# Kernel tuning notes

Measured on AMD Instinct MI355X. Metric: run time of the kernel, lower is better.

The kernel has to match this reference:

```python
import jax, jax.numpy as jnp
import numpy as np
import math

H = 1024
N = 64          # d_state; complex modes = N // 2
N2 = N // 2
B = 8
L = 2048
DT_MIN, DT_MAX = 0.001, 0.1


def setup_inputs() -> dict:
    key = jax.random.key(0)
    ks = jax.random.split(key, 8)
    u = jax.random.normal(ks[0], (B, H, L), dtype=jnp.float32)
    # log_dt ~ Uniform[log(dt_min), log(dt_max)]
    log_dt = (jax.random.uniform(ks[1], (H,), dtype=jnp.float32)
              * (math.log(DT_MAX) - math.log(DT_MIN)) + math.log(DT_MIN))
    # random_dplr with scaling='inverse': real part 0.5, imag = (1/pi)*N*(N/(1+2n)-1)
    n = jnp.arange(N2, dtype=jnp.float32)
    w_real = 0.5 * jnp.ones((1, N2), dtype=jnp.float32)
    w_imag = ((1.0 / math.pi) * N * (N / (1.0 + 2.0 * n) - 1.0))[None, :].astype(jnp.float32)
    log_w_real = jnp.log(w_real + 1e-4)  # module stores log(-w.real + 1e-4)
    # C = randn complex (channels=1, H, N2), scaled by normalized B (folded into randn here)
    C_re = jax.random.normal(ks[2], (1, H, N2), dtype=jnp.float32) / math.sqrt(2 * N2)
    C_im = jax.random.normal(ks[3], (1, H, N2), dtype=jnp.float32) / math.sqrt(2 * N2)
    D = jax.random.normal(ks[4], (1, H), dtype=jnp.float32)
    # output_linear: Conv1d(k=1) from channels*H -> H  => weight (H, H)
    W_out = jax.random.normal(ks[5], (H, H), dtype=jnp.float32) / math.sqrt(H)
    b_out = jax.random.normal(ks[6], (H,), dtype=jnp.float32) * 0.01
    return {"u": u, "log_dt": log_dt, "log_w_real": log_w_real, "w_imag": w_imag,
            "C_re": C_re, "C_im": C_im, "D": D, "W_out": W_out, "b_out": b_out}


def reference(u, log_dt, log_w_real, w_imag, C_re, C_im, D, W_out, b_out):
    b, h, l = u.shape
    # --- SSKernelDiag.forward ---
    dt = jnp.exp(log_dt)                                   # (H,)
    w = -jnp.exp(log_w_real) + 1j * w_imag                 # (n_ssm=1, N2)
    w = jnp.broadcast_to(w, (h, w.shape[-1]))              # repeat copies -> (H, N2)
    dtA = w * dt[:, None]                                  # (H, N2) complex
    C = (C_re + 1j * C_im) * (jnp.exp(dtA) - 1.0) / w      # (c, H, N2)
    # Vandermonde: exp(dtA * arange(L)) -> (H, N2, L) complex
    K = jnp.exp(dtA[:, :, None] * jnp.arange(l, dtype=jnp.float32))
    k = 2.0 * jnp.einsum('chn,hnl->chl', C, K).real        # (c, H, L) float
    # --- FFT convolution ---
    k_f = jnp.fft.rfft(k, n=2 * l)                         # (c, H, L+1)
    u_f = jnp.fft.rfft(u, n=2 * l)                         # (B, H, L+1)
    y_f = jnp.einsum('bhl,chl->bchl', u_f, k_f)
    y = jnp.fft.irfft(y_f, n=2 * l)[..., :l]               # (B, c, H, L)
    # skip connection with D
    y = y + jnp.einsum('bhl,ch->bchl', u, D)
    y = y.reshape(b, -1, l)                                # (B, c*H, L)
    y = jax.nn.gelu(y, approximate=False)
    # output 1x1 conv: (B, c*H, L) x (H, c*H) -> (B, H, L)
    y = jnp.einsum('bil,oi->bol', y, W_out) + b_out[None, :, None]
    return y
```

## Files before the change

### kernel.cpp

```cpp
#include <hip/hip_runtime.h>
#include <hip/hip_bf16.h>

#define HH 1024
#define LL 2048
#define BB 8
#define NN2 32
#define CT 128
#define NCH 16

typedef short bf16x8 __attribute__((ext_vector_type(8)));
typedef float f32x4  __attribute__((ext_vector_type(4)));
typedef float f32x16 __attribute__((ext_vector_type(16)));

static __device__ __forceinline__ unsigned short bfbits(float x) {
    __hip_bfloat16 h = __float2bfloat16(x);
    return *(unsigned short*)&h;
}
static __device__ __forceinline__ float f_from_bits(unsigned short b) {
    __hip_bfloat16 h; *(unsigned short*)&h = b; return __bfloat162float(h);
}
static __device__ __forceinline__ float2 cexp_n(float2 dA, float p) {
    float mag = __expf(dA.x * p);
    float rev = dA.y * p * 0.15915494309f;
    rev -= floorf(rev);
    float ang = rev * 6.28318530718f;
    return make_float2(mag * __cosf(ang), mag * __sinf(ang));
}

#define SWZ(off, row) ((off) ^ (((row) & 7) << 4))

__global__ __launch_bounds__(256) void aux_tables(
    const float* __restrict__ log_dt, const float* __restrict__ log_w_real,
    const float* __restrict__ w_imag, const float* __restrict__ C_re,
    const float* __restrict__ C_im, const float* __restrict__ W,
    __hip_bfloat16* __restrict__ AJ_g, __hip_bfloat16* __restrict__ AP_g,
    float* __restrict__ misc_g, __hip_bfloat16* __restrict__ Wb)
{
    __shared__ float2 dtA_s[NN2];
    __shared__ float2 Cn_s[NN2];
    const int tid = threadIdx.x;
    const int h = blockIdx.x;

    {
        float4 v = ((const float4*)(W + (size_t)h * HH))[tid];
        ushort4 o;
        o.x = bfbits(v.x); o.y = bfbits(v.y); o.z = bfbits(v.z); o.w = bfbits(v.w);
        ((ushort4*)(Wb + (size_t)h * HH))[tid] = o;
    }

    if (tid < NN2) {
        int n = tid;
        float dt = expf(log_dt[h]);
        float wr = -expf(log_w_real[n]);
        float wi = w_imag[n];
        float dar = wr * dt, dai = wi * dt;
        dtA_s[n] = make_float2(dar, dai);
        float er = expf(dar);
        float sn, cs; sincosf(dai, &sn, &cs);
        float exr = er * cs - 1.0f, exi = er * sn;
        float den = wr * wr + wi * wi;
        float fr = (exr * wr + exi * wi) / den;
        float fi = (exi * wr - exr * wi) / den;
        float cre = C_re[h * NN2 + n], cim = C_im[h * NN2 + n];
        float2 Cv = make_float2(cre * fr - cim * fi, cre * fi + cim * fr);
        Cn_s[n] = Cv;
        misc_g[h * 256 + 128 + 2 * n]     = Cv.x;
        misc_g[h * 256 + 128 + 2 * n + 1] = Cv.y;
        float magA = expf(dar * 128.0f);
        float snA, csA; sincosf(dai * 128.0f, &snA, &csA);
        misc_g[h * 256 + 192 + 2 * n]     = magA * csA;
        misc_g[h * 256 + 192 + 2 * n + 1] = magA * snA;
    }
    __syncthreads();

    char* ajb = (char*)AJ_g + (size_t)h * 16384;
    #pragma unroll
    for (int q = 0; q < 2; ++q) {
        int task = q * 256 + tid;
        int n = task >> 4, j0 = (task & 15) * 8;
        float2 dA = dtA_s[n];
        unsigned rw[4], iw[4];
        #pragma unroll
        for (int i2 = 0; i2 < 4; ++i2) {
            float2 a0 = cexp_n(dA, (float)(127 - j0 - 2 * i2));
            float2 a1 = cexp_n(dA, (float)(127 - j0 - 2 * i2 - 1));
            rw[i2] = (unsigned)bfbits(a0.x) | ((unsigned)bfbits(a1.x) << 16);
            iw[i2] = (unsigned)bfbits(a0.y) | ((unsigned)bfbits(a1.y) << 16);
        }
        int r0 = 2 * n, r1 = 2 * n + 1;
        *(uint4*)(ajb + SWZ(r0 * 256 + j0 * 2, r0)) = make_uint4(rw[0], rw[1], rw[2], rw[3]);
        *(uint4*)(ajb + SWZ(r1 * 256 + j0 * 2, r1)) = make_uint4(iw[0], iw[1], iw[2], iw[3]);
    }

    char* apb = (char*)AP_g + (size_t)h * 16384;
    #pragma unroll
    for (int q = 0; q < 2; ++q) {
        int task = q * 256 + tid;
        int ttr = task >> 2, n0 = (task & 3) * 8;
        unsigned w[8];
        #pragma unroll
        for (int i = 0; i < 8; ++i) {
            float2 a = cexp_n(dtA_s[n0 + i], (float)(ttr + 1));
            w[i] = (unsigned)bfbits(2.0f * a.x) | ((unsigned)bfbits(-2.0f * a.y) << 16);
        }
        *(uint4*)(apb + SWZ(ttr * 128 + n0 * 4, ttr))      = make_uint4(w[0], w[1], w[2], w[3]);
        *(uint4*)(apb + SWZ(ttr * 128 + n0 * 4 + 16, ttr)) = make_uint4(w[4], w[5], w[6], w[7]);
    }

    {
        int t = tid >> 1, nb = (tid & 1) * 16;
        float s = 0.f;
        #pragma unroll
        for (int i = 0; i < 16; ++i) {
            int n = nb + i;
            float2 a = cexp_n(dtA_s[n], (float)t);
            float2 C = Cn_s[n];
            s += C.x * a.x - C.y * a.y;
        }
        s += __shfl_xor(s, 1);
        if ((tid & 1) == 0) misc_g[h * 256 + t] = 2.0f * s;
    }
}

#define S_U    0
#define S_UN   16384
#define S_P    32768
#define S_KT   40960
#define S_KTP  41984
#define S_TOT  46208

__global__ __launch_bounds__(512, 6) void ssm_mfma(
    const float* __restrict__ u,
    const __hip_bfloat16* __restrict__ AJ_g,
    const __hip_bfloat16* __restrict__ AP_g,
    const float* __restrict__ misc_g,
    const float* __restrict__ Dp, __hip_bfloat16* __restrict__ g_out)
{
    extern __shared__ char smem[];
    float*  kt   = (float*)(smem + S_KT);
    float2* CnL  = (float2*)(smem + S_KT + 512);
    float2* A128 = (float2*)(smem + S_KT + 768);

    const int tid  = threadIdx.x;
    const int lane = tid & 63;
    const int wave = tid >> 6;
    const int wm   = wave >> 2;
    const int wn   = wave & 3;
    const int h    = blockIdx.x;
    const int bh   = blockIdx.y;

    {
        const char* ajs = (const char*)AJ_g + (size_t)h * 16384;
        __builtin_amdgcn_global_load_lds(
            (const __attribute__((address_space(1))) void*)(ajs + tid * 16),
            (__attribute__((address_space(3))) void*)(smem + S_UN + wave * 1024), 16, 0, 0);
        __builtin_amdgcn_global_load_lds(
            (const __attribute__((address_space(1))) void*)(ajs + 8192 + tid * 16),
            (__attribute__((address_space(3))) void*)(smem + S_UN + 8192 + wave * 1024), 16, 0, 0);
        if (tid < 64) {
            const char* ms = (const char*)misc_g + (size_t)h * 1024;
            __builtin_amdgcn_global_load_lds(
                (const __attribute__((address_space(1))) void*)(ms + tid * 16),
                (__attribute__((address_space(3))) void*)(smem + S_KT), 16, 0, 0);
        }
    }

    float4 ureg[4];
    #pragma unroll
    for (int q = 0; q < 4; ++q) {
        int b = bh * 4 + q;
        ureg[q] = *(const float4*)(u + ((size_t)(b * HH + h)) * LL + tid * 4);
    }
    #pragma unroll
    for (int q = 0; q < 4; ++q) {
        int row = q * 16 + (tid >> 5);
        int j   = (tid & 31) * 4;
        ushort4 o;
        o.x = bfbits(ureg[q].x); o.y = bfbits(ureg[q].y);
        o.z = bfbits(ureg[q].z); o.w = bfbits(ureg[q].w);
        *(ushort4*)(smem + SWZ(S_U + row * 256 + j * 2, row)) = o;
    }
    asm volatile("s_waitcnt vmcnt(0)" ::: "memory");
    __syncthreads();

    {
        int s = wave;
        int i0 = lane * 4;
        ushort4 o;
        #pragma unroll
        for (int k = 0; k < 4; ++k) {
            int src = 127 - s - (i0 + k);
            ((unsigned short*)&o)[k] = (src >= 0) ? bfbits(kt[src]) : (unsigned short)0;
        }
        *(ushort4*)(smem + S_KTP + s * 528 + i0 * 2) = o;
        if (lane < 2) {
            *(ushort4*)(smem + S_KTP + s * 528 + 512 + lane * 8) = make_ushort4(0, 0, 0, 0);
        }
    }

    f32x4 accP[2] = {};
    #pragma unroll
    for (int ks = 0; ks < 4; ++ks) {
        int kf = ks * 32 + (lane >> 4) * 8;
        bf16x8 a0, a1, b0;
        {
            int r = wm * 32 + (lane & 15);
            a0 = *(bf16x8*)(smem + SWZ(S_U + r * 256 + kf * 2, r));
            int r2 = r + 16;
            a1 = *(bf16x8*)(smem + SWZ(S_U + r2 * 256 + kf * 2, r2));
        }
        {
            int r = wn * 16 + (lane & 15);
            b0 = *(bf16x8*)(smem + SWZ(S_UN + r * 256 + kf * 2, r));
        }
        accP[0] = __builtin_amdgcn_mfma_f32_16x16x32_bf16(a0, b0, accP[0], 0, 0, 0);
        accP[1] = __builtin_amdgcn_mfma_f32_16x16x32_bf16(a1, b0, accP[1], 0, 0, 0);
    }
    #pragma unroll
    for (int mt = 0; mt < 2; ++mt)
        #pragma unroll
        for (int r = 0; r < 4; ++r) {
            int row = wm * 32 + mt * 16 + (lane >> 4) * 4 + r;
            int col = wn * 16 + (lane & 15);
            *(unsigned short*)(smem + SWZ(S_P + row * 128 + col * 2, row)) =
                bfbits(accP[mt][r]);
        }
    __syncthreads();

    {
        const char* aps = (const char*)AP_g + (size_t)h * 16384;
        __builtin_amdgcn_global_load_lds(
            (const __attribute__((address_space(1))) void*)(aps + tid * 16),
            (__attribute__((address_space(3))) void*)(smem + S_UN + wave * 1024), 16, 0, 0);
        __builtin_amdgcn_global_load_lds(
            (const __attribute__((address_space(1))) void*)(aps + 8192 + tid * 16),
            (__attribute__((address_space(3))) void*)(smem + S_UN + 8192 + wave * 1024), 16, 0, 0);
    }

    if (tid < 128) {
        int b = tid >> 5, n = tid & 31;
        float2 C = CnL[n];
        float2 A = A128[n];
        unsigned int pv[NCH];
        int offs[NCH];
        #pragma unroll
        for (int c = 0; c < NCH; ++c) {
            int row = b * 16 + c;
            offs[c] = SWZ(S_P + row * 128 + n * 4, row);
            pv[c] = *(unsigned int*)(smem + offs[c]);
        }
        float sr = 0.f, si = 0.f;
        #pragma unroll
        for (int c = 0; c < NCH; ++c) {
            float pr = f_from_bits((unsigned short)(pv[c] & 0xffff));
            float pi = f_from_bits((unsigned short)(pv[c] >> 16));
            float csr = C.x * sr - C.y * si;
            float csi = C.x * si + C.y * sr;
            *(unsigned int*)(smem + offs[c]) =
                (unsigned)bfbits(csr) | ((unsigned)bfbits(csi) << 16);
            float nsr = A.x * sr - A.y * si + pr;
            float nsi = A.x * si + A.y * sr + pi;
            sr = nsr; si = nsi;
        }
    }

    f32x4 acc[2][2] = {};
    #pragma unroll
    for (int ks = 0; ks < 4; ++ks) {
        int kf = ks * 32 + (lane >> 4) * 8;
        bf16x8 a0, a1, bv[2];
        {
            int r = wm * 32 + (lane & 15);
            a0 = *(bf16x8*)(smem + SWZ(S_U + r * 256 + kf * 2, r));
            int r2 = r + 16;
            a1 = *(bf16x8*)(smem + SWZ(S_U + r2 * 256 + kf * 2, r2));
        }
        #pragma unroll
        for (int nt = 0; nt < 2; ++nt) {
            int ttr = wn * 32 + nt * 16 + (lane & 15);
            int s   = (127 - ttr) & 7;
            int gq  = (127 - ttr + kf) >> 3;
            bv[nt] = *(bf16x8*)(smem + S_KTP + s * 528 + gq * 16);
        }
        #pragma unroll
        for (int nt = 0; nt < 2; ++nt) {
            acc[0][nt] = __builtin_amdgcn_mfma_f32_16x16x32_bf16(a0, bv[nt], acc[0][nt], 0, 0, 0);
            acc[1][nt] = __builtin_amdgcn_mfma_f32_16x16x32_bf16(a1, bv[nt], acc[1][nt], 0, 0, 0);
        }
    }
    asm volatile("s_waitcnt vmcnt(0)" ::: "memory");
    __syncthreads();

    #pragma unroll
    for (int ks = 0; ks < 2; ++ks) {
        int kf = ks * 32 + (lane >> 4) * 8;
        bf16x8 a0, a1, bv[2];
        {
            int r = wm * 32 + (lane & 15);
            a0 = *(bf16x8*)(smem + SWZ(S_P + r * 128 + kf * 2, r));
            int r2 = r + 16;
            a1 = *(bf16x8*)(smem + SWZ(S_P + r2 * 128 + kf * 2, r2));
        }
        #pragma unroll
        for (int nt = 0; nt < 2; ++nt) {
            int ttr = wn * 32 + nt * 16 + (lane & 15);
            bv[nt] = *(bf16x8*)(smem + SWZ(S_UN + ttr * 128 + kf * 2, ttr));
        }
        #pragma unroll
        for (int nt = 0; nt < 2; ++nt) {
            acc[0][nt] = __builtin_amdgcn_mfma_f32_16x16x32_bf16(a0, bv[nt], acc[0][nt], 0, 0, 0);
            acc[1][nt] = __builtin_amdgcn_mfma_f32_16x16x32_bf16(a1, bv[nt], acc[1][nt], 0, 0, 0);
        }
    }

    const float Dv = Dp[h];
    #pragma unroll
    for (int mt = 0; mt < 2; ++mt)
        #pragma unroll
        for (int nt = 0; nt < 2; ++nt)
            #pragma unroll
            for (int r = 0; r < 4; ++r) {
                int row = wm * 32 + mt * 16 + (lane >> 4) * 4 + r;
                int ttr = wn * 32 + nt * 16 + (lane & 15);
                int off = SWZ(S_U + row * 256 + ttr * 2, row);
                float uv = f_from_bits(*(unsigned short*)(smem + off));
                float y = acc[mt][nt][r] + Dv * uv;
                float z = 0.7978845608f * (y + 0.044715f * y * y * y);
                float e = __expf(2.0f * z);
                float th = 1.0f - 2.0f / (e + 1.0f);
                float gel = 0.5f * y * (1.0f + th);
                *(unsigned short*)(smem + off) = bfbits(gel);
            }
    __syncthreads();
    #pragma unroll
    for (int q = 0; q < 2; ++q) {
        int flat = q * 512 + tid;
        int row = flat >> 4, c16 = flat & 15;
        uint4 v = *(uint4*)(smem + SWZ(S_U + row * 256 + c16 * 16, row));
        int b = bh * 4 + (row >> 4), c = row & 15;
        *(uint4*)(g_out + ((size_t)(b * HH + h)) * LL + c * CT + c16 * 8) = v;
    }
}

__global__ __launch_bounds__(256) void transpose_g(
    const __hip_bfloat16* __restrict__ g, __hip_bfloat16* __restrict__ gT)
{
    __shared__ __hip_bfloat16 t[64][66];
    const int tid = threadIdx.x;
    const int b  = blockIdx.z;
    const int h0 = blockIdx.x * 64;
    const int l0 = blockIdx.y * 64;

    #pragma unroll
    for (int q = 0; q < 2; ++q) {
        int idx = tid + q * 256;
        int r = idx >> 3, c8 = (idx & 7) * 8;
        uint4 v = *(const uint4*)(g + ((size_t)(b * HH + h0 + r)) * LL + l0 + c8);
        unsigned int* dst = (unsigned int*)&t[r][c8];
        dst[0] = v.x; dst[1] = v.y; dst[2] = v.z; dst[3] = v.w;
    }
    __syncthreads();
    #pragma unroll
    for (int q = 0; q < 2; ++q) {
        int idx = tid + q * 256;
        int r = idx >> 3, c8 = (idx & 7) * 8;
        unsigned short tmp[8];
        #pragma unroll
        for (int j = 0; j < 8; ++j) tmp[j] = *(unsigned short*)&t[c8 + j][r];
        uint4 o;
        o.x = (unsigned)tmp[0] | ((unsigned)tmp[1] << 16);
        o.y = (unsigned)tmp[2] | ((unsigned)tmp[3] << 16);
        o.z = (unsigned)tmp[4] | ((unsigned)tmp[5] << 16);
        o.w = (unsigned)tmp[6] | ((unsigned)tmp[7] << 16);
        *(uint4*)(gT + ((size_t)(b * LL + l0 + r)) * HH + h0 + c8) = o;
    }
}

#define GSLOT 32768
#define STAGE_TILE(kt_, s_)                                                      \
    {                                                                            \
        const int k0_ = (kt_) * 64;                                              \
        _Pragma("unroll")                                                        \
        for (int v_ = 0; v_ < 4; ++v_) {                                         \
            int row_ = v_ * 64 + rsub;                                           \
            const __hip_bfloat16* ga_ = Wb + (size_t)(o0 + row_) * HH + k0_ + csw; \
            const __hip_bfloat16* gb_ = gT + (size_t)(n0 + row_) * HH + k0_ + csw; \
            char* dA_ = smem + (s_) * GSLOT + (v_ * 64 + wave * 8) * 128;        \
            char* dB_ = smem + 2 * GSLOT + (s_) * GSLOT + (v_ * 64 + wave * 8) * 128; \
            __builtin_amdgcn_global_load_lds(                                    \
                (const __attribute__((address_space(1))) void*)ga_,              \
                (__attribute__((address_space(3))) void*)dA_, 16, 0, 0);         \
            __builtin_amdgcn_global_load_lds(                                    \
                (const __attribute__((address_space(1))) void*)gb_,              \
                (__attribute__((address_space(3))) void*)dB_, 16, 0, 0);         \
        }                                                                        \
    }

#define COMPUTE_TILE(s_)                                                         \
    {                                                                            \
        const char* baseA = smem + (s_) * GSLOT;                                 \
        const char* baseB = smem + 2 * GSLOT + (s_) * GSLOT;                     \
        _Pragma("unroll")                                                        \
        for (int ks = 0; ks < 4; ++ks) {                                         \
            int kf = ks * 16 + (lane >> 5) * 8;                                  \
            bf16x8 af[4], bfv[2];                                                \
            _Pragma("unroll")                                                    \
            for (int mt = 0; mt < 4; ++mt) {                                     \
                int ra = wm * 128 + mt * 32 + (lane & 31);                       \
                int c  = kf ^ ((ra & 7) << 3);                                   \
                af[mt] = *(const bf16x8*)(baseA + ra * 128 + c * 2);             \
            }                                                                    \
            _Pragma("unroll")                                                    \
            for (int nt = 0; nt < 2; ++nt) {                                     \
                int rb = wn * 64 + nt * 32 + (lane & 31);                        \
                int c  = kf ^ ((rb & 7) << 3);                                   \
                bfv[nt] = *(const bf16x8*)(baseB + rb * 128 + c * 2);            \
            }                                                                    \
            _Pragma("unroll")                                                    \
            for (int mt = 0; mt < 4; ++mt)                                       \
                _Pragma("unroll")                                                \
                for (int nt = 0; nt < 2; ++nt)                                   \
                    acc[mt][nt] = __builtin_amdgcn_mfma_f32_32x32x16_bf16(       \
                        af[mt], bfv[nt], acc[mt][nt], 0, 0, 0);                  \
        }                                                                        \
    }

__global__ __launch_bounds__(512, 2) void out_gemm_256(
    const __hip_bfloat16* __restrict__ Wb,
    const __hip_bfloat16* __restrict__ gT,
    const float* __restrict__ bias,
    float* __restrict__ out)
{
    extern __shared__ char smem[];
    const int tid  = threadIdx.x;
    const int lane = tid & 63;
    const int wave = tid >> 6;
    const int wm = wave >> 2;
    const int wn = wave & 3;

    int wg  = blockIdx.x;
    int swz = (wg & 7) * 32 + (wg >> 3);
    const int o0 = (swz & 3) * 256;
    const int n0 = (swz >> 2) * 256;

    const int rsub = tid >> 3;
    const int csw  = ((tid & 7) ^ (rsub & 7)) << 3;

    f32x16 acc[4][2] = {};

    STAGE_TILE(0, 0)
    STAGE_TILE(1, 1)

    for (int t = 0; t < 15; ++t) {
        asm volatile("s_waitcnt vmcnt(8)" ::: "memory");
        __builtin_amdgcn_s_barrier();
        COMPUTE_TILE(t & 1)
        asm volatile("s_waitcnt lgkmcnt(0)" ::: "memory");
        __builtin_amdgcn_s_barrier();
        if (t < 14) STAGE_TILE(t + 2, t & 1)
    }
    asm volatile("s_waitcnt vmcnt(0)" ::: "memory");
    __builtin_amdgcn_s_barrier();
    COMPUTE_TILE(1)

    const int bb = n0 >> 11;
    #pragma unroll
    for (int mt = 0; mt < 4; ++mt) {
        int obase = o0 + wm * 128 + mt * 32 + 4 * (lane >> 5);
        #pragma unroll
        for (int nt = 0; nt < 2; ++nt) {
            int l = (n0 + wn * 64 + nt * 32 + (lane & 31)) & 2047;
            #pragma unroll
            for (int reg = 0; reg < 16; ++reg) {
                int o = obase + (reg & 3) + 8 * (reg >> 2);
                out[((size_t)(bb * HH + o)) * LL + l] = acc[mt][nt][reg] + bias[o];
            }
        }
    }
}

extern "C" void kernel_launch(void* const* d_in, const int* in_sizes, int n_in,
                              void* d_out, int out_size, void* d_ws, size_t ws_size,
                              hipStream_t stream) {
    const float* u          = (const float*)d_in[0];
    const float* log_dt     = (const float*)d_in[1];
    const float* log_w_real = (const float*)d_in[2];
    const float* w_imag     = (const float*)d_in[3];
    const float* C_re       = (const float*)d_in[4];
    const float* C_im       = (const float*)d_in[5];
    const float* Dp         = (const float*)d_in[6];
    const float* W          = (const float*)d_in[7];
    const float* bias       = (const float*)d_in[8];
    float* out = (float*)d_out;

    __hip_bfloat16* AJ_g = (__hip_bfloat16*)d_out;
    __hip_bfloat16* AP_g = (__hip_bfloat16*)((char*)d_out + 16777216);
    __hip_bfloat16* g    = (__hip_bfloat16*)((char*)d_out + 33554432);
    __hip_bfloat16* gT     = (__hip_bfloat16*)d_ws;
    __hip_bfloat16* Wb     = (__hip_bfloat16*)((char*)d_ws + 33554432);
    float*          misc_g = (float*)((char*)d_ws + 35651584);

    hipFuncSetAttribute((const void*)ssm_mfma,
                        hipFuncAttributeMaxDynamicSharedMemorySize, S_TOT);
    hipFuncSetAttribute((const void*)out_gemm_256,
                        hipFuncAttributeMaxDynamicSharedMemorySize, 131072);

    aux_tables<<<dim3(HH), 256, 0, stream>>>(log_dt, log_w_real, w_imag,
                                             C_re, C_im, W, AJ_g, AP_g, misc_g, Wb);
    ssm_mfma<<<dim3(HH, 2), 512, S_TOT, stream>>>(u, AJ_g, AP_g, misc_g, Dp, g);
    transpose_g<<<dim3(HH / 64, LL / 64, BB), 256, 0, stream>>>(g, gT);
    out_gemm_256<<<dim3(256), 512, 131072, stream>>>(Wb, gT, bias, out);
}
```

Before: 101.9 us.

## Move GELU into transpose and restructure output GEMM into quadrant-pipelined 16x16 MFMA

GELU moves out of the SSM kernel's epilogue and into the transpose kernel, so the SSM kernel writes the pre-activation value. The output GEMM drops 32x32x16 MFMAs in favour of 16x16x32 ones and splits each 256x256 tile into four quadrants. Staging of the next K-tile's A/B halves is interleaved between quadrant MFMA phases with finer vmcnt waits. The aim is to overlap global-to-LDS loads with compute and to ease SSM-kernel work. The cost is more barriers per tile and a different register footprint, since the launch bound drops its min-blocks hint and may cut occupancy.

```diff
diff --git a/kernel.cpp b/kernel.cpp
--- a/kernel.cpp
+++ b/kernel.cpp
@@ -10,7 +10,6 @@
 
 typedef short bf16x8 __attribute__((ext_vector_type(8)));
 typedef float f32x4  __attribute__((ext_vector_type(4)));
-typedef float f32x16 __attribute__((ext_vector_type(16)));
 
 static __device__ __forceinline__ unsigned short bfbits(float x) {
     __hip_bfloat16 h = __float2bfloat16(x);
@@ -25,6 +24,11 @@
     rev -= floorf(rev);
     float ang = rev * 6.28318530718f;
     return make_float2(mag * __cosf(ang), mag * __sinf(ang));
+}
+static __device__ __forceinline__ float gelu_f(float y) {
+    float z = 0.7978845608f * (y + 0.044715f * y * y * y);
+    float e = __expf(2.0f * z);
+    return 0.5f * y * (1.0f + (1.0f - 2.0f / (e + 1.0f)));
 }
 
 #define SWZ(off, row) ((off) ^ (((row) & 7) << 4))
@@ -325,11 +329,7 @@
                 int off = SWZ(S_U + row * 256 + ttr * 2, row);
                 float uv = f_from_bits(*(unsigned short*)(smem + off));
                 float y = acc[mt][nt][r] + Dv * uv;
-                float z = 0.7978845608f * (y + 0.044715f * y * y * y);
-                float e = __expf(2.0f * z);
-                float th = 1.0f - 2.0f / (e + 1.0f);
-                float gel = 0.5f * y * (1.0f + th);
-                *(unsigned short*)(smem + off) = bfbits(gel);
+                *(unsigned short*)(smem + off) = bfbits(y);
             }
     __syncthreads();
     #pragma unroll
@@ -357,7 +357,14 @@
         int r = idx >> 3, c8 = (idx & 7) * 8;
         uint4 v = *(const uint4*)(g + ((size_t)(b * HH + h0 + r)) * LL + l0 + c8);
         unsigned int* dst = (unsigned int*)&t[r][c8];
-        dst[0] = v.x; dst[1] = v.y; dst[2] = v.z; dst[3] = v.w;
+        unsigned int* src = (unsigned int*)&v;
+        #pragma unroll
+        for (int w = 0; w < 4; ++w) {
+            unsigned int pw = src[w];
+            float a = gelu_f(f_from_bits((unsigned short)(pw & 0xffff)));
+            float c = gelu_f(f_from_bits((unsigned short)(pw >> 16)));
+            dst[w] = (unsigned)bfbits(a) | ((unsigned)bfbits(c) << 16);
+        }
     }
     __syncthreads();
     #pragma unroll
@@ -376,56 +383,99 @@
     }
 }
 
-#define GSLOT 32768
-#define STAGE_TILE(kt_, s_)                                                      \
+#define QSLOT 65536
+
+#define STAGE_A_HALF(kt_, s_, h_)                                                \
     {                                                                            \
         const int k0_ = (kt_) * 64;                                              \
         _Pragma("unroll")                                                        \
-        for (int v_ = 0; v_ < 4; ++v_) {                                         \
+        for (int v2_ = 0; v2_ < 2; ++v2_) {                                      \
+            int v_ = (h_) * 2 + v2_;                                             \
             int row_ = v_ * 64 + rsub;                                           \
             const __hip_bfloat16* ga_ = Wb + (size_t)(o0 + row_) * HH + k0_ + csw; \
-            const __hip_bfloat16* gb_ = gT + (size_t)(n0 + row_) * HH + k0_ + csw; \
-            char* dA_ = smem + (s_) * GSLOT + (v_ * 64 + wave * 8) * 128;        \
-            char* dB_ = smem + 2 * GSLOT + (s_) * GSLOT + (v_ * 64 + wave * 8) * 128; \
+            char* dA_ = smem + (s_) * QSLOT + (v_ * 64 + wave * 8) * 128;        \
             __builtin_amdgcn_global_load_lds(                                    \
                 (const __attribute__((address_space(1))) void*)ga_,              \
                 (__attribute__((address_space(3))) void*)dA_, 16, 0, 0);         \
+        }                                                                        \
+    }
+
+#define STAGE_B_HALF(kt_, s_, h_)                                                \
+    {                                                                            \
+        const int k0_ = (kt_) * 64;                                              \
+        _Pragma("unroll")                                                        \
+        for (int v2_ = 0; v2_ < 2; ++v2_) {                                      \
+            int v_ = (h_) * 2 + v2_;                                             \
+            int row_ = v_ * 64 + rsub;                                           \
+            const __hip_bfloat16* gb_ = gT + (size_t)(n0 + row_) * HH + k0_ + csw; \
+            char* dB_ = smem + (s_) * QSLOT + 32768 + (v_ * 64 + wave * 8) * 128; \
             __builtin_amdgcn_global_load_lds(                                    \
                 (const __attribute__((address_space(1))) void*)gb_,              \
                 (__attribute__((address_space(3))) void*)dB_, 16, 0, 0);         \
         }                                                                        \
     }
 
-#define COMPUTE_TILE(s_)                                                         \
+#define READ_A(af_, qa_)                                                         \
+    _Pragma("unroll")                                                            \
+    for (int mt = 0; mt < 2; ++mt)                                               \
+        _Pragma("unroll")                                                        \
+        for (int ks = 0; ks < 2; ++ks) {                                         \
+            int ra = (qa_) * 128 + wm4 * 32 + mt * 16 + (lane & 15);             \
+            int c  = (ks * 32 + (lane >> 4) * 8) ^ ((ra & 7) << 3);              \
+            af_[mt][ks] = *(const bf16x8*)(baseA + ra * 128 + c * 2);            \
+        }
+
+#define READ_B(bf_, qb_)                                                         \
+    _Pragma("unroll")                                                            \
+    for (int nt = 0; nt < 4; ++nt)                                               \
+        _Pragma("unroll")                                                        \
+        for (int ks = 0; ks < 2; ++ks) {                                         \
+            int rb = (qb_) * 128 + wn2 * 64 + nt * 16 + (lane & 15);             \
+            int c  = (ks * 32 + (lane >> 4) * 8) ^ ((rb & 7) << 3);              \
+            bf_[nt][ks] = *(const bf16x8*)(baseB + rb * 128 + c * 2);            \
+        }
+
+#define DO_MFMA(qa_, qb_, af_, bf_)                                              \
+    _Pragma("unroll")                                                            \
+    for (int mt = 0; mt < 2; ++mt)                                               \
+        _Pragma("unroll")                                                        \
+        for (int nt = 0; nt < 4; ++nt) {                                         \
+            acc[qa_][qb_][mt][nt] = __builtin_amdgcn_mfma_f32_16x16x32_bf16(     \
+                af_[mt][0], bf_[nt][0], acc[qa_][qb_][mt][nt], 0, 0, 0);         \
+            acc[qa_][qb_][mt][nt] = __builtin_amdgcn_mfma_f32_16x16x32_bf16(     \
+                af_[mt][1], bf_[nt][1], acc[qa_][qb_][mt][nt], 0, 0, 0);         \
+        }
+
+#define TILE_BODY(t_, s_, W0, W1, W2, DOSTAGE)                                   \
     {                                                                            \
-        const char* baseA = smem + (s_) * GSLOT;                                 \
-        const char* baseB = smem + 2 * GSLOT + (s_) * GSLOT;                     \
-        _Pragma("unroll")                                                        \
-        for (int ks = 0; ks < 4; ++ks) {                                         \
-            int kf = ks * 16 + (lane >> 5) * 8;                                  \
-            bf16x8 af[4], bfv[2];                                                \
-            _Pragma("unroll")                                                    \
-            for (int mt = 0; mt < 4; ++mt) {                                     \
-                int ra = wm * 128 + mt * 32 + (lane & 31);                       \
-                int c  = kf ^ ((ra & 7) << 3);                                   \
-                af[mt] = *(const bf16x8*)(baseA + ra * 128 + c * 2);             \
-            }                                                                    \
-            _Pragma("unroll")                                                    \
-            for (int nt = 0; nt < 2; ++nt) {                                     \
-                int rb = wn * 64 + nt * 32 + (lane & 31);                        \
-                int c  = kf ^ ((rb & 7) << 3);                                   \
-                bfv[nt] = *(const bf16x8*)(baseB + rb * 128 + c * 2);            \
-            }                                                                    \
-            _Pragma("unroll")                                                    \
-            for (int mt = 0; mt < 4; ++mt)                                       \
-                _Pragma("unroll")                                                \
-                for (int nt = 0; nt < 2; ++nt)                                   \
-                    acc[mt][nt] = __builtin_amdgcn_mfma_f32_32x32x16_bf16(       \
-                        af[mt], bfv[nt], acc[mt][nt], 0, 0, 0);                  \
-        }                                                                        \
-    }
-
-__global__ __launch_bounds__(512, 2) void out_gemm_256(
+        const char* baseA = smem + (s_) * QSLOT;                                 \
+        const char* baseB = smem + (s_) * QSLOT + 32768;                         \
+        bf16x8 af0[2][2], af1[2][2], bf[4][2];                                   \
+                                                    \
+        asm volatile("s_waitcnt vmcnt(" #W0 ")" ::: "memory");                   \
+        __builtin_amdgcn_s_barrier();                                            \
+        if (DOSTAGE) STAGE_A_HALF((t_) + 1, (s_) ^ 1, 0)                         \
+        READ_A(af0, 0)                                                           \
+        READ_B(bf, 0)                                                            \
+        DO_MFMA(0, 0, af0, bf)                                                   \
+                                                    \
+        asm volatile("s_waitcnt vmcnt(" #W1 ")" ::: "memory");                   \
+        __builtin_amdgcn_s_barrier();                                            \
+        if (DOSTAGE) STAGE_B_HALF((t_) + 1, (s_) ^ 1, 0)                         \
+        READ_A(af1, 1)                                                           \
+        DO_MFMA(1, 0, af1, bf)                                                   \
+                                                    \
+        asm volatile("s_waitcnt vmcnt(" #W2 ")" ::: "memory");                   \
+        __builtin_amdgcn_s_barrier();                                            \
+        if (DOSTAGE) STAGE_A_HALF((t_) + 1, (s_) ^ 1, 1)                         \
+        READ_B(bf, 1)                                                            \
+        DO_MFMA(1, 1, af1, bf)                                                   \
+              \
+        if (DOSTAGE) STAGE_B_HALF((t_) + 1, (s_) ^ 1, 1)                         \
+        DO_MFMA(0, 1, af0, bf)                                                   \
+    }
+
+__global__ __launch_bounds__(512) void out_gemm_256p(
     const __hip_bfloat16* __restrict__ Wb,
     const __hip_bfloat16* __restrict__ gT,
     const float* __restrict__ bias,
@@ -435,8 +485,8 @@
     const int tid  = threadIdx.x;
     const int lane = tid & 63;
     const int wave = tid >> 6;
-    const int wm = wave >> 2;
-    const int wn = wave & 3;
+    const int wm4 = wave >> 1;
+    const int wn2 = wave & 1;
 
     int wg  = blockIdx.x;
     int swz = (wg & 7) * 32 + (wg >> 3);
@@ -446,37 +496,37 @@
     const int rsub = tid >> 3;
     const int csw  = ((tid & 7) ^ (rsub & 7)) << 3;
 
-    f32x16 acc[4][2] = {};
-
-    STAGE_TILE(0, 0)
-    STAGE_TILE(1, 1)
+    f32x4 acc[2][2][2][4] = {};
+
+    STAGE_A_HALF(0, 0, 0)
+    STAGE_B_HALF(0, 0, 0)
+    STAGE_A_HALF(0, 0, 1)
+    STAGE_B_HALF(0, 0, 1)
 
     for (int t = 0; t < 15; ++t) {
-        asm volatile("s_waitcnt vmcnt(8)" ::: "memory");
-        __builtin_amdgcn_s_barrier();
-        COMPUTE_TILE(t & 1)
-        asm volatile("s_waitcnt lgkmcnt(0)" ::: "memory");
-        __builtin_amdgcn_s_barrier();
-        if (t < 14) STAGE_TILE(t + 2, t & 1)
-    }
-    asm volatile("s_waitcnt vmcnt(0)" ::: "memory");
-    __builtin_amdgcn_s_barrier();
-    COMPUTE_TILE(1)
-
-    const int bb = n0 >> 11;
-    #pragma unroll
-    for (int mt = 0; mt < 4; ++mt) {
-        int obase = o0 + wm * 128 + mt * 32 + 4 * (lane >> 5);
-        #pragma unroll
-        for (int nt = 0; nt < 2; ++nt) {
-            int l = (n0 + wn * 64 + nt * 32 + (lane & 31)) & 2047;
+        TILE_BODY(t, (t & 1), 4, 4, 4, 1)
+    }
+    TILE_BODY(15, 1, 4, 2, 0, 0)
+
+    const int bb  = n0 >> 11;
+    const int l0g = n0 & 2047;
+    #pragma unroll
+    for (int qa = 0; qa < 2; ++qa)
+        #pragma unroll
+        for (int mt = 0; mt < 2; ++mt)
             #pragma unroll
-            for (int reg = 0; reg < 16; ++reg) {
-                int o = obase + (reg & 3) + 8 * (reg >> 2);
-                out[((size_t)(bb * HH + o)) * LL + l] = acc[mt][nt][reg] + bias[o];
+            for (int r = 0; r < 4; ++r) {
+                int o = o0 + qa * 128 + wm4 * 32 + mt * 16 + (lane >> 4) * 4 + r;
+                float bo = bias[o];
+                #pragma unroll
+                for (int qb = 0; qb < 2; ++qb)
+                    #pragma unroll
+                    for (int nt = 0; nt < 4; ++nt) {
+                        int l = l0g + qb * 128 + wn2 * 64 + nt * 16 + (lane & 15);
+                        out[((size_t)(bb * HH + o)) * LL + l] =
+                            acc[qa][qb][mt][nt][r] + bo;
+                    }
             }
-        }
-    }
 }
 
 extern "C" void kernel_launch(void* const* d_in, const int* in_sizes, int n_in,
@@ -502,12 +552,12 @@
 
     hipFuncSetAttribute((const void*)ssm_mfma,
                         hipFuncAttributeMaxDynamicSharedMemorySize, S_TOT);
-    hipFuncSetAttribute((const void*)out_gemm_256,
+    hipFuncSetAttribute((const void*)out_gemm_256p,
                         hipFuncAttributeMaxDynamicSharedMemorySize, 131072);
 
     aux_tables<<<dim3(HH), 256, 0, stream>>>(log_dt, log_w_real, w_imag,
                                              C_re, C_im, W, AJ_g, AP_g, misc_g, Wb);
     ssm_mfma<<<dim3(HH, 2), 512, S_TOT, stream>>>(u, AJ_g, AP_g, misc_g, Dp, g);
     transpose_g<<<dim3(HH / 64, LL / 64, BB), 256, 0, stream>>>(g, gT);
-    out_gemm_256<<<dim3(256), 512, 131072, stream>>>(Wb, gT, bias, out);
-}
+    out_gemm_256p<<<dim3(256), 512, 131072, stream>>>(Wb, gT, bias, out);
+}
```

After: 96.19 us. -5.6%, faster.
